# Performance work log

Hardware: AMD Instinct MI355X
Metric: run time of the kernel (lower is better)

Reference implementation:

```python
import jax, jax.numpy as jnp
import numpy as np

IMG_H, IMG_W = 512.0, 512.0
PRED_SIZES = [(64, 64), (32, 32), (16, 16), (8, 8), (4, 4), (2, 2)]
ASPECT_RATIOS = [1.0, 2.0, 0.5, 3.0]
SCALES = [0.04, 0.1, 0.26, 0.42, 0.58, 0.74]
N_CLASSES = 21
CONF_THRESH = 0.01
IOU_THRESH = 0.45
TOP_K = 100
NMS_MAX = 200
XY_VAR, WH_VAR = 0.1, 0.2
NEG = -1e30  # stand-in for -inf that is safe under autodiff


def generate_boxes():
    # Standard SSD anchors (cx, cy, w, h), normalized to [0, 1].
    all_boxes = []
    for (fh, fw), s in zip(PRED_SIZES, SCALES):
        cx = (np.arange(fw, dtype=np.float32) + 0.5) / fw
        cy = (np.arange(fh, dtype=np.float32) + 0.5) / fh
        cxg, cyg = np.meshgrid(cx, cy)  # [fh, fw]
        for ar in ASPECT_RATIOS:
            w = s * np.sqrt(ar)
            h = s / np.sqrt(ar)
            b = np.stack([cxg, cyg, np.full_like(cxg, w), np.full_like(cxg, h)], axis=-1)
            all_boxes.append(b.reshape(-1, 4))
    return np.concatenate(all_boxes, axis=0).astype(np.float32)  # [21840, 4]


def setup_inputs() -> dict:
    key = jax.random.key(0)
    n_boxes = sum(fh * fw for fh, fw in PRED_SIZES) * len(ASPECT_RATIOS)
    y_pred = jax.random.normal(key, (32, n_boxes, N_CLASSES + 4), dtype=jnp.float32)
    box_tensor = jnp.asarray(generate_boxes())
    return {"y_pred": y_pred, "box_tensor": box_tensor}


def _decode(y_pred, box_tensor):
    # y_pred: [B, N, C+4], box_tensor: [N, 4] (cx, cy, w, h)
    logits = y_pred[..., :-4]
    class_ids = jnp.argmax(logits, axis=-1).astype(jnp.float32)  # [B, N]
    confidences = jnp.max(logits, axis=-1)                       # [B, N]
    a_cx, a_cy, a_w, a_h = box_tensor[:, 0], box_tensor[:, 1], box_tensor[:, 2], box_tensor[:, 3]
    cx = y_pred[..., -4] * XY_VAR * a_w + a_cx
    cy = y_pred[..., -3] * XY_VAR * a_h + a_cy
    w = jnp.exp(y_pred[..., -2] * WH_VAR) * a_w
    h = jnp.exp(y_pred[..., -1] * WH_VAR) * a_h
    xmin = jnp.clip(cx - 0.5 * w, 0.0, 1.0)
    ymin = jnp.clip(cy - 0.5 * h, 0.0, 1.0)
    xmax = jnp.clip(cx + 0.5 * w, 0.0, 1.0)
    ymax = jnp.clip(cy + 0.5 * h, 0.0, 1.0)
    # [B, N, 6]: class_id, confidence, xmin, ymin, xmax, ymax
    return jnp.stack([class_ids, confidences, xmin, ymin, xmax, ymax], axis=-1)


def _nms_image(preds):
    # preds: [N, 6]. Greedy NMS over confident, non-background boxes, then top-k.
    N = preds.shape[0]
    valid = (preds[:, 0] != 0.0) & (preds[:, 1] > CONF_THRESH)
    scores0 = jnp.where(valid, preds[:, 1], NEG)
    boxes = preds[:, 2:6]  # xmin, ymin, xmax, ymax
    areas = (boxes[:, 2] - boxes[:, 0]) * (boxes[:, 3] - boxes[:, 1])
    idxs = jnp.arange(N)

    def step(scores, _):
        i = jnp.argmax(scores)
        best = scores[i]
        ok = best > NEG * 0.5
        b = boxes[i]
        ix1 = jnp.maximum(b[0], boxes[:, 0])
        iy1 = jnp.maximum(b[1], boxes[:, 1])
        ix2 = jnp.minimum(b[2], boxes[:, 2])
        iy2 = jnp.minimum(b[3], boxes[:, 3])
        inter = jnp.maximum(ix2 - ix1, 0.0) * jnp.maximum(iy2 - iy1, 0.0)
        union = areas[i] + areas - inter
        iou = jnp.where(union > 0.0, inter / jnp.maximum(union, 1e-12), 0.0)
        suppress = (iou > IOU_THRESH) | (idxs == i)
        new_scores = jnp.where(ok & suppress, NEG, scores)
        row = jnp.where(ok, preds[i], 0.0)         # zero-pad like the TF pad path
        s = jnp.where(ok, best, 0.0)               # pad rows get score 0
        return new_scores, (row, s)

    _, (rows, sel_scores) = jax.lax.scan(step, scores0, None, length=NMS_MAX)
    # rows: [NMS_MAX, 6] in descending score order; top_k like the TF layer.
    _, ti = jax.lax.top_k(sel_scores, TOP_K)
    return rows[ti]  # [TOP_K, 6]


def reference(y_pred, box_tensor):
    preds = _decode(y_pred, box_tensor)          # [B, N, 6]
    return jax.vmap(_nms_image)(preds)           # [B, TOP_K, 6]
```

## Files before the change

### kernel.cpp

```cpp
#include <hip/hip_runtime.h>
#include <math.h>

typedef unsigned long long ull;
typedef unsigned int uint;

#define NBOX 21840
#define SEGSZ 512
#define NSEG 44
#define NPAD (NSEG*SEGSZ)
#define PFXS 23
#define OUTW 24
#define NWALK (NSEG*PFXS)
#define MCAP 1024
#define WIN 512
#define BATCH 32
#define NCLS 21
#define NEGV -1e30f
#define MIOU (15099494.5/33554432.0)

__device__ __forceinline__ uint key_hi(float s) {
    uint b = __float_as_uint(s);
    uint m = (uint)((int)b >> 31) | 0x80000000u;
    return ~(b ^ m);
}
__device__ __forceinline__ float key_score(uint hi) {
    uint srt = ~hi;
    uint b = (srt & 0x80000000u) ? (srt ^ 0x80000000u) : ~srt;
    return __uint_as_float(b);
}

__device__ __forceinline__ float area_of(float4 b) {
    return __fmul_rn(__fsub_rn(b.z, b.x), __fsub_rn(b.w, b.y));
}
__device__ __forceinline__ bool sup_check(float4 a, float aarea, float4 c, float carea) {
    float ix1 = fmaxf(a.x, c.x), iy1 = fmaxf(a.y, c.y);
    float ix2 = fminf(a.z, c.z), iy2 = fminf(a.w, c.w);
    float inter = __fmul_rn(fmaxf(__fsub_rn(ix2, ix1), 0.f), fmaxf(__fsub_rn(iy2, iy1), 0.f));
    float uni = __fsub_rn(__fadd_rn(aarea, carea), inter);
    return (uni > 0.f) && ((double)inter > MIOU * (double)fmaxf(uni, 1e-12f));
}

__device__ __forceinline__ ull cex_shfl(ull v, int j, bool asc, int lane) {
    ull pv = __shfl_xor(v, j);
    bool keepmin = (((lane & j) == 0) == asc);
    bool less = (v < pv);
    return (keepmin == less) ? v : pv;
}

__global__ __launch_bounds__(512) void decode_sort_kernel(
    const float* __restrict__ y_pred, const float* __restrict__ box_tensor,
    float4* __restrict__ BX, ull* __restrict__ KS, ull* __restrict__ KS2)
{
    __shared__ float st[SEGSZ * 25];
    __shared__ ull sk[SEGSZ];
    int img = blockIdx.y, seg = blockIdx.x, tid = threadIdx.x;
    int b0 = seg * SEGSZ;
    int nval = NBOX - b0; nval = nval < 0 ? 0 : (nval > SEGSZ ? SEGSZ : nval);
    if (nval > 0) {
        const float* src = y_pred + ((size_t)img * NBOX + b0) * 25;
        int nf = nval * 25, nf4 = nf >> 2;
        const float4* src4 = (const float4*)src;
        float4* st4 = (float4*)st;
        for (int f = tid; f < nf4; f += 512) st4[f] = src4[f];
        for (int f = (nf4 << 2) + tid; f < nf; f += 512) st[f] = src[f];
    }
    __syncthreads();
    int i = b0 + tid;
    size_t o = (size_t)img * NPAD + i;
    ull v;
    if (tid < nval) {
        const float* yl = st + tid * 25;
        float best = yl[0]; int bi = 0;
        #pragma unroll
        for (int k = 1; k < NCLS; k++) { float x = yl[k]; if (x > best) { best = x; bi = k; } }
        float4 a = ((const float4*)box_tensor)[i];
        float t0 = yl[21], t1 = yl[22], t2 = yl[23], t3 = yl[24];
        float cx = __fadd_rn(__fmul_rn(__fmul_rn(t0, 0.1f), a.z), a.x);
        float cy = __fadd_rn(__fmul_rn(__fmul_rn(t1, 0.1f), a.w), a.y);
        float w  = __fmul_rn((float)exp((double)__fmul_rn(t2, 0.2f)), a.z);
        float h  = __fmul_rn((float)exp((double)__fmul_rn(t3, 0.2f)), a.w);
        float hw = __fmul_rn(0.5f, w), hh = __fmul_rn(0.5f, h);
        float xmin = fminf(fmaxf(__fsub_rn(cx, hw), 0.f), 1.f);
        float ymin = fminf(fmaxf(__fsub_rn(cy, hh), 0.f), 1.f);
        float xmax = fminf(fmaxf(__fadd_rn(cx, hw), 0.f), 1.f);
        float ymax = fminf(fmaxf(__fadd_rn(cy, hh), 0.f), 1.f);
        bool valid = (bi != 0) && (best > 0.01f);
        BX[o] = make_float4(xmin, ymin, xmax, ymax);
        uint hi = valid ? key_hi(best) : __float_as_uint(NEGV);
        v = ((ull)hi << 32) | ((uint)(i << 8)) | (uint)bi;
    } else {
        v = ((ull)__float_as_uint(NEGV) << 32) | ((uint)(i << 8));
    }
    int lane = tid & 63;
    for (int k = 2; k <= SEGSZ; k <<= 1) {
        for (int j = k >> 1; j >= 64; j >>= 1) {
            sk[tid] = v; __syncthreads();
            ull pv = sk[tid ^ j];
            bool keepmin = (((tid & j) == 0) == ((tid & k) == 0));
            bool less = (v < pv);
            v = (keepmin == less) ? v : pv;
            __syncthreads();
        }
        int j0 = (k >> 1) < 32 ? (k >> 1) : 32;
        for (int j = j0; j >= 1; j >>= 1)
            v = cex_shfl(v, j, (tid & k) == 0, lane);
    }
    KS[(size_t)img * NPAD + b0 + tid] = v;
    if (tid < OUTW) KS2[(size_t)img * (NSEG * OUTW) + seg * OUTW + tid] = v;
}

__global__ __launch_bounds__(512) void nms_kernel(
    const ull* __restrict__ KS2, const ull* __restrict__ KS,
    const float4* __restrict__ BX, float* __restrict__ out)
{
    __shared__ ull klist[MCAP];
    __shared__ float4 cbox[WIN];
    __shared__ ull scol[WIN];
    __shared__ float4 accbox[100];
    __shared__ float  accarea[100];
    __shared__ ull pref[NSEG];

    int img = blockIdx.x, tid = threadIdx.x;
    int wid = tid >> 6, lane = tid & 63;
    const ull* ks2i = KS2 + (size_t)img * (NSEG * OUTW);
    const float4* BXg = BX + (size_t)img * NPAD;

    ull v[2];
    #pragma unroll
    for (int r = 0; r < 2; r++) {
        int e = (wid << 7) + (r << 6) + lane;
        v[r] = (e < NWALK) ? ks2i[(e / PFXS) * OUTW + (e % PFXS)] : ~0ull;
    }
    if (tid < NSEG) pref[tid] = ks2i[tid * OUTW + PFXS];

    for (int k = 2; k <= MCAP; k <<= 1) {
        if ((k >> 1) >= 128) {
            #pragma unroll
            for (int r = 0; r < 2; r++) klist[(wid << 7) + (r << 6) + lane] = v[r];
            for (int j = k >> 1; j >= 128; j >>= 1) {
                __syncthreads();
                int t = tid;
                int i = ((t & ~(j - 1)) << 1) | (t & (j - 1));
                int l = i | j;
                ull a = klist[i], b = klist[l];
                if ((a > b) == ((i & k) == 0)) { klist[i] = b; klist[l] = a; }
            }
            __syncthreads();
            #pragma unroll
            for (int r = 0; r < 2; r++) v[r] = klist[(wid << 7) + (r << 6) + lane];
        }
        if ((k >> 1) >= 64) {
            int e = (wid << 7) + lane;
            bool asc = ((e & k) == 0);
            ull a = v[0], b = v[1];
            if ((a > b) == asc) { v[0] = b; v[1] = a; }
        }
        int j0 = (k >> 1) < 32 ? (k >> 1) : 32;
        for (int j = j0; j >= 1; j >>= 1) {
            #pragma unroll
            for (int r = 0; r < 2; r++) {
                int e = (wid << 7) + (r << 6) + lane;
                v[r] = cex_shfl(v[r], j, (e & k) == 0, lane);
            }
        }
    }
    #pragma unroll
    for (int r = 0; r < 2; r++) klist[(wid << 7) + (r << 6) + lane] = v[r];
    __syncthreads();

    {
        int c = (wid << 6) + lane;
        ull k = klist[c];
        float4 bx = BXg[((uint)k) >> 8];
        cbox[c] = bx;
        float myar = area_of(bx);
        ull col = 0;
        #pragma unroll 4
        for (int i = 0; i < 64; i++) {
            float4 ib = cbox[(wid << 6) + i];
            bool s = (i < lane) && sup_check(ib, area_of(ib), bx, myar);
            col |= ((ull)s) << i;
        }
        scol[c] = col;
    }
    __syncthreads();

    if (tid >= 64) return;
    float* orow = out + (size_t)img * 600;
    const ull* ksg = KS + (size_t)img * NPAD;

    ull cutk = ~0ull;
    for (int s = 0; s < NSEG; s++) { ull x = pref[s]; if (x < cutk) cutk = x; }

    int A = 0, stop = 0, done = 0;
    int acc0 = 0, acc1 = 0;

    for (int base = 0; base < WIN && !stop; base += 64) {
        int c = base + lane;
        ull kk = klist[c];
        float4 bb = cbox[c];
        float ca = area_of(bb);
        ull mycol = scol[c];
        bool valid = !(kk >> 63) && (kk < cutk);
        ull vmask = __ballot(valid);
        bool alive = valid;
        for (int a = 0; a < A; a++)
            alive = alive & !sup_check(accbox[a], accarea[a], bb, ca);
        ull m = __ballot(alive);
        while (m && A < 100) {
            int i = __ffsll(m) - 1;
            if (lane == i) { accbox[A] = bb; accarea[A] = ca; }
            if (lane == (A & 63)) { if (A < 64) acc0 = base + i; else acc1 = base + i; }
            A++;
            m &= ~(1ull << i);
            m &= __ballot(!((mycol >> i) & 1ull));
        }
        if (A >= 100) { stop = 1; done = 1; }
        else if (vmask != ~0ull) {
            stop = 1;
            int fi = __ffsll(~vmask) - 1;
            ull fk = __shfl(kk, fi);
            done = (fk >= cutk) ? (int)(cutk >> 63) : 1;
        }
        __builtin_amdgcn_wave_barrier();
    }

    int accW = A;
    if (lane < accW) {
        ull k = klist[acc0]; float4 b = cbox[acc0];
        float* o = orow + lane * 6;
        o[0] = (float)((uint)k & 0xffu); o[1] = key_score((uint)(k >> 32));
        o[2] = b.x; o[3] = b.y; o[4] = b.z; o[5] = b.w;
    }
    if (64 + lane < accW) {
        ull k = klist[acc1]; float4 b = cbox[acc1];
        float* o = orow + (64 + lane) * 6;
        o[0] = (float)((uint)k & 0xffu); o[1] = key_score((uint)(k >> 32));
        o[2] = b.x; o[3] = b.y; o[4] = b.z; o[5] = b.w;
    }

    if (!stop) {
        for (int base = WIN; base < MCAP && !stop; base += 64) {
            int pos = base + lane;
            ull kk = klist[pos];
            bool valid = !(kk >> 63) && (kk < cutk);
            ull vmask = __ballot(valid);
            float4 bb = BXg[((uint)kk) >> 8];
            float ca = area_of(bb);
            bool alive = valid;
            for (int a = 0; a < A; a++)
                alive = alive & !sup_check(accbox[a], accarea[a], bb, ca);
            ull cand = __ballot(alive);
            while (cand && A < 100) {
                int i = __ffsll(cand) - 1;
                float4 ib = make_float4(__shfl(bb.x, i), __shfl(bb.y, i),
                                        __shfl(bb.z, i), __shfl(bb.w, i));
                float ia = __shfl(ca, i);
                ull row = __ballot(sup_check(ib, ia, bb, ca));
                if (lane == i) {
                    accbox[A] = bb; accarea[A] = ca;
                    float* o = orow + A * 6;
                    o[0] = (float)((uint)kk & 0xffu); o[1] = key_score((uint)(kk >> 32));
                    o[2] = bb.x; o[3] = bb.y; o[4] = bb.z; o[5] = bb.w;
                }
                A++;
                cand &= ~(1ull << i);
                cand &= ~row;
            }
            if (A >= 100) { stop = 1; done = 1; }
            else if (vmask != ~0ull) {
                stop = 1;
                int fi = __ffsll(~vmask) - 1;
                ull fk = __shfl(kk, fi);
                done = (fk >= cutk) ? (int)(cutk >> 63) : 1;
            }
            __builtin_amdgcn_wave_barrier();
        }
        if (!stop) done = (int)(cutk >> 63);
    }

    if (!done && A < 100) {
        ull nextk = cutk;
        while (A < 100) {
            ull best = ~0ull;
            for (int e = lane; e < NPAD; e += 64) {
                ull kk2 = ksg[e];
                if (kk2 >= nextk && kk2 < best) best = kk2;
            }
            #pragma unroll
            for (int off = 32; off; off >>= 1) {
                ull oo = __shfl_xor(best, off);
                if (oo < best) best = oo;
            }
            if (best >> 63) break;
            uint bhi = (uint)(best >> 32), blo = (uint)best;
            float4 cb = BXg[blo >> 8];
            float ca2 = area_of(cb);
            bool sup2 = false;
            #pragma unroll
            for (int t = 0; t < 2; t++) {
                int slot = lane + 64 * t;
                if (slot < A && sup_check(accbox[slot], accarea[slot], cb, ca2)) sup2 = true;
            }
            if (__ballot(sup2) == 0ull) {
                if (lane == 0) {
                    accbox[A] = cb; accarea[A] = ca2;
                    float* o = orow + A * 6;
                    o[0] = (float)(blo & 0xffu); o[1] = key_score(bhi);
                    o[2] = cb.x; o[3] = cb.y; o[4] = cb.z; o[5] = cb.w;
                }
                A++;
            }
            nextk = best + 1;
            __builtin_amdgcn_wave_barrier();
        }
    }

    for (int r = lane; r < (100 - A) * 6; r += 64) orow[A * 6 + r] = 0.f;
}

extern "C" void kernel_launch(void* const* d_in, const int* in_sizes, int n_in,
                              void* d_out, int out_size, void* d_ws, size_t ws_size,
                              hipStream_t stream)
{
    const float* y_pred     = (const float*)d_in[0];
    const float* box_tensor = (const float*)d_in[1];
    float* out = (float*)d_out;

    size_t stride = (size_t)BATCH * NPAD;
    ull*    KS  = (ull*)d_ws;
    float4* BX  = (float4*)(KS + stride);
    ull*    KS2 = (ull*)(BX + stride);

    decode_sort_kernel<<<dim3(NSEG, BATCH), 512, 0, stream>>>(y_pred, box_tensor, BX, KS, KS2);
    nms_kernel<<<BATCH, 512, 0, stream>>>(KS2, KS, BX, out);
}
```

Measured before the change: 143.5 us.

## Replace full segment bitonic sort with per-wave sort plus top-24 merge

Instead of fully bitonic-sorting all 512 keys per segment through shared memory with many block barriers, each wave sorts its 64 keys with shuffles and keeps its top 24. A single wave then sorts the 192 candidates and writes the segment's top 24 to KS2. KS now holds unsorted keys in original order, which changes a layout contract with nms_kernel that may depend on KS being sorted per segment.

```diff
diff --git a/kernel.cpp b/kernel.cpp
--- a/kernel.cpp
+++ b/kernel.cpp
@@ -52,8 +52,9 @@
     float4* __restrict__ BX, ull* __restrict__ KS, ull* __restrict__ KS2)
 {
     __shared__ float st[SEGSZ * 25];
-    __shared__ ull sk[SEGSZ];
+    __shared__ ull mbuf[8 * 24];
     int img = blockIdx.y, seg = blockIdx.x, tid = threadIdx.x;
+    int wid = tid >> 6, lane = tid & 63;
     int b0 = seg * SEGSZ;
     int nval = NBOX - b0; nval = nval < 0 ? 0 : (nval > SEGSZ ? SEGSZ : nval);
     if (nval > 0) {
@@ -91,22 +92,52 @@
     } else {
         v = ((ull)__float_as_uint(NEGV) << 32) | ((uint)(i << 8));
     }
-    int lane = tid & 63;
-    for (int k = 2; k <= SEGSZ; k <<= 1) {
-        for (int j = k >> 1; j >= 64; j >>= 1) {
-            sk[tid] = v; __syncthreads();
-            ull pv = sk[tid ^ j];
-            bool keepmin = (((tid & j) == 0) == ((tid & k) == 0));
-            bool less = (v < pv);
-            v = (keepmin == less) ? v : pv;
-            __syncthreads();
+    KS[o] = v;
+
+    for (int k = 2; k <= 64; k <<= 1) {
+        bool asc = (k == 64) || ((lane & k) == 0);
+        for (int j = k >> 1; j >= 1; j >>= 1)
+            v = cex_shfl(v, j, asc, lane);
+    }
+    if (lane < 24) mbuf[wid * 24 + lane] = v;
+    __syncthreads();
+
+    if (wid != 0) return;
+
+    ull m[4];
+    #pragma unroll
+    for (int r = 0; r < 4; r++) {
+        int e = (r << 6) + lane;
+        m[r] = (e < 192) ? mbuf[e] : ~0ull;
+    }
+    for (int k = 2; k <= 256; k <<= 1) {
+        #pragma unroll
+        for (int jr = 2; jr >= 1; jr >>= 1) {
+            int j = jr << 6;
+            if ((k >> 1) >= j) {
+                #pragma unroll
+                for (int r = 0; r < 4; r++) {
+                    if ((r & jr) == 0) {
+                        int rh = r | jr;
+                        int e = (r << 6) + lane;
+                        bool asc = ((e & k) == 0) || (k == 256);
+                        ull a = m[r], b = m[rh];
+                        if ((a > b) == asc) { m[r] = b; m[rh] = a; }
+                    }
+                }
+            }
         }
         int j0 = (k >> 1) < 32 ? (k >> 1) : 32;
-        for (int j = j0; j >= 1; j >>= 1)
-            v = cex_shfl(v, j, (tid & k) == 0, lane);
-    }
-    KS[(size_t)img * NPAD + b0 + tid] = v;
-    if (tid < OUTW) KS2[(size_t)img * (NSEG * OUTW) + seg * OUTW + tid] = v;
+        for (int j = j0; j >= 1; j >>= 1) {
+            #pragma unroll
+            for (int r = 0; r < 4; r++) {
+                int e = (r << 6) + lane;
+                bool asc = ((e & k) == 0) || (k == 256);
+                m[r] = cex_shfl(m[r], j, asc, lane);
+            }
+        }
+    }
+    if (lane < OUTW) KS2[(size_t)img * (NSEG * OUTW) + seg * OUTW + lane] = m[0];
 }
 
 __global__ __launch_bounds__(512) void nms_kernel(
```

Result: faster. 139.6 us (-2.7%).
